# Performance work log

Hardware: AMD Instinct MI355X
Metric: run time of the kernel (lower is better)

The kernel has to match this reference:

```python
import jax, jax.numpy as jnp
import numpy as np

B, T, D, H = 32, 2048, 1024, 128


def setup_inputs() -> dict:
    key = jax.random.key(0)
    ks = jax.random.split(key, 7)
    s = 1.0 / np.sqrt(D)
    return {
        "x": jax.random.normal(ks[0], (B, T, D), dtype=jnp.float32),
        "Wk": jax.random.normal(ks[1], (D, H), dtype=jnp.float32) * s,
        "bk": jax.random.normal(ks[2], (H,), dtype=jnp.float32) * 0.01,
        "Wq": jax.random.normal(ks[3], (D, H), dtype=jnp.float32) * s,
        "bq": jax.random.normal(ks[4], (H,), dtype=jnp.float32) * 0.01,
        "Wv": jax.random.normal(ks[5], (D, H), dtype=jnp.float32) * s,
        "bv": jax.random.normal(ks[6], (H,), dtype=jnp.float32) * 0.01,
    }


def reference(x, Wk, bk, Wq, bq, Wv, bv):
    # Single causal attention head. NOTE faithful quirk: scores = K @ Q^T.
    k = x @ Wk + bk  # [B,T,H]
    q = x @ Wq + bq  # [B,T,H]
    v = x @ Wv + bv  # [B,T,H]
    scale = k.shape[-1] ** -0.5
    wei = jnp.einsum("bth,bsh->bts", k, q) * scale  # [B,T,T], K on the left
    t = x.shape[1]
    causal = jnp.tril(jnp.ones((t, t), dtype=bool))
    wei = jnp.where(causal, wei, -jnp.inf)
    wei = jax.nn.softmax(wei, axis=-1)
    # dropout is eval-mode identity (deterministic reference)
    out = jnp.einsum("bts,bsh->bth", wei, v)  # [B,T,H]
    return out
```

## Files before the change

kernel.cpp:

```cpp
#include <hip/hip_runtime.h>
#include <hip/hip_bf16.h>
#include <stdint.h>

typedef __bf16 bf16;
typedef __bf16 bf16x8 __attribute__((ext_vector_type(8)));
typedef __bf16 bf16x4 __attribute__((ext_vector_type(4)));
typedef float f32x4 __attribute__((ext_vector_type(4)));

#define BB 32
#define TT 2048
#define DD 1024
#define HH 128
#define SCALE 0.08838834764831845f
#define LOG2E 1.4426950408889634f

__device__ __forceinline__ void gl_lds16(const bf16* g, bf16* l) {
  __builtin_amdgcn_global_load_lds((__attribute__((address_space(1))) const void*)g,
                                   (__attribute__((address_space(3))) void*)l,
                                   16, 0, 0);
}

__global__ __launch_bounds__(256) void prep_w(const float* __restrict__ Wk,
                                              const float* __restrict__ Wq,
                                              const float* __restrict__ Wv,
                                              bf16* __restrict__ Wt) {
  int tid = blockIdx.x * 256 + threadIdx.x;
  int mat = tid >> 14;
  int r = tid & 16383;
  int h = r & 127;
  int d0 = (r >> 7) << 3;
  const float* W = (mat == 0) ? Wk : (mat == 1) ? Wq : Wv;
  bf16x8 v;
#pragma unroll
  for (int i = 0; i < 8; ++i) v[i] = (bf16)W[(size_t)(d0 + i) * HH + h];
  *(bf16x8*)(Wt + ((size_t)mat * HH + h) * DD + d0) = v;
}

__global__ __launch_bounds__(256) void qkv_proj(
    const float* __restrict__ x, const bf16* __restrict__ Wt,
    const float* __restrict__ bk, const float* __restrict__ bq,
    const float* __restrict__ bv,
    bf16* __restrict__ kb, bf16* __restrict__ qb, bf16* __restrict__ Vt) {
  const int bid = blockIdx.x;
  const int mat = bid % 3;
  const int mtile = bid / 3;
  const int tid = threadIdx.x;
  const int lane = tid & 63;
  const int w = tid >> 6;
  const int wr = w >> 1, wc = w & 1;
  const int l15 = lane & 15, l4 = lane >> 4;

  __shared__ __attribute__((aligned(16))) bf16 As[2][128][40];
  __shared__ __attribute__((aligned(16))) bf16 Bs[2][128][40];

  const size_t row0 = (size_t)mtile * 128;
  const bf16* Wm = Wt + (size_t)mat * HH * DD;
  const float* bias = (mat == 0) ? bk : (mat == 1) ? bq : bv;

  const int ar = tid >> 3, ac = (tid & 7) * 4;
  const int br = tid >> 2, bc = (tid & 3) * 8;

  f32x4 acc[4][4];
#pragma unroll
  for (int i = 0; i < 4; ++i)
#pragma unroll
    for (int j = 0; j < 4; ++j) acc[i][j] = f32x4{0.f, 0.f, 0.f, 0.f};

  auto stage = [&](int buf, int k0) {
#pragma unroll
    for (int p = 0; p < 4; ++p) {
      int r = p * 32 + ar;
      f32x4 a = *(const f32x4*)(x + (row0 + r) * DD + k0 + ac);
      bf16x4 t;
#pragma unroll
      for (int i = 0; i < 4; ++i) t[i] = (bf16)a[i];
      *(bf16x4*)&As[buf][r][ac] = t;
    }
#pragma unroll
    for (int p = 0; p < 2; ++p) {
      int r = p * 64 + br;
      bf16x8 bv8 = *(const bf16x8*)(Wm + (size_t)r * DD + k0 + bc);
      *(bf16x8*)&Bs[buf][r][bc] = bv8;
    }
  };

  stage(0, 0);
  __syncthreads();

  for (int k0 = 0; k0 < DD; k0 += 32) {
    const int cur = (k0 >> 5) & 1;
    if (k0 + 32 < DD) stage(cur ^ 1, k0 + 32);

    bf16x8 af[4], bfr[4];
#pragma unroll
    for (int f = 0; f < 4; ++f)
      af[f] = *(const bf16x8*)&As[cur][wr * 64 + f * 16 + l15][l4 * 8];
#pragma unroll
    for (int f = 0; f < 4; ++f)
      bfr[f] = *(const bf16x8*)&Bs[cur][wc * 64 + f * 16 + l15][l4 * 8];
#pragma unroll
    for (int i = 0; i < 4; ++i)
#pragma unroll
      for (int j = 0; j < 4; ++j)
        acc[i][j] = __builtin_amdgcn_mfma_f32_16x16x32_bf16(af[i], bfr[j],
                                                            acc[i][j], 0, 0, 0);
    __syncthreads();
  }

  float bvv[4];
#pragma unroll
  for (int f = 0; f < 4; ++f) bvv[f] = bias[wc * 64 + f * 16 + l15];

  if (mat == 2) {
    const int bidx = mtile >> 4;
    const int tbase = (mtile & 15) * 128;
#pragma unroll
    for (int i = 0; i < 4; ++i)
#pragma unroll
      for (int j = 0; j < 4; ++j) {
        int col = wc * 64 + j * 16 + l15;
        bf16x4 v4;
#pragma unroll
        for (int e = 0; e < 4; ++e) v4[e] = (bf16)(acc[i][j][e] + bvv[j]);
        int t = tbase + wr * 64 + i * 16 + l4 * 4;
        *(bf16x4*)(Vt + ((size_t)bidx * HH + col) * TT + t) = v4;
      }
  } else {
    const float ks = (mat == 0) ? (SCALE * LOG2E) : 1.0f;
    bf16* outp = (mat == 0) ? kb : qb;
#pragma unroll
    for (int i = 0; i < 4; ++i)
#pragma unroll
      for (int j = 0; j < 4; ++j) {
        int col = wc * 64 + j * 16 + l15;
#pragma unroll
        for (int e = 0; e < 4; ++e) {
          int row = wr * 64 + i * 16 + l4 * 4 + e;
          outp[(row0 + row) * HH + col] = (bf16)((acc[i][j][e] + bvv[j]) * ks);
        }
      }
  }
}

__global__ __launch_bounds__(256, 3) void attn(const bf16* __restrict__ kb,
                                               const bf16* __restrict__ qb,
                                               const bf16* __restrict__ Vt,
                                               float* __restrict__ out) {
  const int bid = blockIdx.x;
  const int b = bid & 31;
  const int p = bid >> 5;
  const int tid = threadIdx.x;
  const int lane = tid & 63;
  const int w = tid >> 6;
  const int l15 = lane & 15, l4 = lane >> 4;

  __shared__ __attribute__((aligned(16))) bf16 Es[64 * 128];
  __shared__ __attribute__((aligned(16))) bf16 Vs[128 * 64];
  __shared__ __attribute__((aligned(16))) bf16 Ps[4][16 * 72];

  for (int job = 0; job < 2; ++job) {
    const int tile = job ? p : (31 - p);
    const int t0 = tile * 64;

    bf16x8 af[4];
    {
      const bf16* kp = kb + ((size_t)b * TT + t0 + w * 16 + l15) * HH + l4 * 8;
#pragma unroll
      for (int kc = 0; kc < 4; ++kc) af[kc] = *(const bf16x8*)(kp + kc * 32);
    }

    f32x4 o[8];
#pragma unroll
    for (int j = 0; j < 8; ++j) o[j] = f32x4{0.f, 0.f, 0.f, 0.f};
    float mrow[4], lrow[4];
#pragma unroll
    for (int e = 0; e < 4; ++e) { mrow[e] = -1e30f; lrow[e] = 0.f; }

    const int nst = tile + 1;
    for (int jt = 0; jt < nst; ++jt) {
      const int s0 = jt * 64;
      {
        const bf16* Eg = qb + ((size_t)b * TT + s0) * HH;
#pragma unroll
        for (int it = 0; it < 4; ++it) {
          int L = w * 256 + it * 64 + lane;
          int er = L >> 4, ec = L & 15;
          int ecs = ec ^ (er & 7);
          gl_lds16(Eg + er * HH + ecs * 8, Es + (size_t)(w * 256 + it * 64) * 8);
        }
        const bf16* Vg = Vt + (size_t)b * HH * TT + s0;
#pragma unroll
        for (int it = 0; it < 4; ++it) {
          int L = w * 256 + it * 64 + lane;
          int vr = L >> 3, vc = L & 7;
          int vcs = vc ^ (vr & 7);
          gl_lds16(Vg + (size_t)vr * TT + vcs * 8, Vs + (size_t)(w * 256 + it * 64) * 8);
        }
      }
      __syncthreads();

      f32x4 s[4];
#pragma unroll
      for (int j = 0; j < 4; ++j) s[j] = f32x4{0.f, 0.f, 0.f, 0.f};
#pragma unroll
      for (int kc = 0; kc < 4; ++kc) {
        bf16x8 ef[4];
#pragma unroll
        for (int fn = 0; fn < 4; ++fn) {
          int er = fn * 16 + l15;
          int c = kc * 4 + l4;
          int cs = c ^ (er & 7);
          ef[fn] = *(const bf16x8*)&Es[er * 128 + cs * 8];
        }
#pragma unroll
        for (int fn = 0; fn < 4; ++fn)
          s[fn] = __builtin_amdgcn_mfma_f32_16x16x32_bf16(af[kc], ef[fn],
                                                          s[fn], 0, 0, 0);
      }

      if (s0 + 63 > t0 + w * 16) {
#pragma unroll
        for (int fn = 0; fn < 4; ++fn)
#pragma unroll
          for (int e = 0; e < 4; ++e) {
            int tg = t0 + w * 16 + l4 * 4 + e;
            int sg = s0 + fn * 16 + l15;
            if (sg > tg) s[fn][e] = -1e30f;
          }
      }

      float mx[4];
#pragma unroll
      for (int e = 0; e < 4; ++e) {
        float m = fmaxf(fmaxf(s[0][e], s[1][e]), fmaxf(s[2][e], s[3][e]));
#pragma unroll
        for (int d = 1; d < 16; d <<= 1) m = fmaxf(m, __shfl_xor(m, d));
        mx[e] = m;
      }
      float g = fmaxf(fmaxf(mx[0] - mrow[0], mx[1] - mrow[1]),
                      fmaxf(mx[2] - mrow[2], mx[3] - mrow[3]));
      if (!__all(g <= 8.0f)) {
#pragma unroll
        for (int e = 0; e < 4; ++e) {
          float mn = fmaxf(mrow[e], mx[e]);
          float rsc = exp2f(mrow[e] - mn);
          lrow[e] *= rsc;
#pragma unroll
          for (int fh = 0; fh < 8; ++fh) o[fh][e] *= rsc;
          mrow[e] = mn;
        }
      }
#pragma unroll
      for (int e = 0; e < 4; ++e) {
        float ps = 0.f;
#pragma unroll
        for (int fn = 0; fn < 4; ++fn) {
          float pv = exp2f(s[fn][e] - mrow[e]);
          s[fn][e] = pv;
          ps += pv;
        }
#pragma unroll
        for (int d = 1; d < 16; d <<= 1) ps += __shfl_xor(ps, d);
        lrow[e] += ps;
      }

#pragma unroll
      for (int fn = 0; fn < 4; ++fn)
#pragma unroll
        for (int e = 0; e < 4; ++e)
          Ps[w][(l4 * 4 + e) * 72 + fn * 16 + l15] = (bf16)s[fn][e];

#pragma unroll
      for (int kc = 0; kc < 2; ++kc) {
        bf16x8 pf = *(const bf16x8*)&Ps[w][l15 * 72 + kc * 32 + l4 * 8];
#pragma unroll
        for (int fh = 0; fh < 8; ++fh) {
          int vr = fh * 16 + l15;
          int c = kc * 4 + l4;
          int cs = c ^ (vr & 7);
          bf16x8 vf = *(const bf16x8*)&Vs[vr * 64 + cs * 8];
          o[fh] = __builtin_amdgcn_mfma_f32_16x16x32_bf16(pf, vf, o[fh], 0, 0, 0);
        }
      }
      __syncthreads();
    }

#pragma unroll
    for (int e = 0; e < 4; ++e) {
      float rl = 1.0f / lrow[e];
      int tg = t0 + w * 16 + l4 * 4 + e;
#pragma unroll
      for (int fh = 0; fh < 8; ++fh)
        out[((size_t)b * TT + tg) * HH + fh * 16 + l15] = o[fh][e] * rl;
    }
  }
}

extern "C" void kernel_launch(void* const* d_in, const int* in_sizes, int n_in,
                              void* d_out, int out_size, void* d_ws, size_t ws_size,
                              hipStream_t stream) {
  (void)in_sizes; (void)n_in; (void)out_size; (void)ws_size;
  const float* x  = (const float*)d_in[0];
  const float* Wk = (const float*)d_in[1];
  const float* bk = (const float*)d_in[2];
  const float* Wq = (const float*)d_in[3];
  const float* bq = (const float*)d_in[4];
  const float* Wv = (const float*)d_in[5];
  const float* bv = (const float*)d_in[6];
  float* out = (float*)d_out;

  const size_t NTH = (size_t)BB * TT * HH;
  bf16* kb = (bf16*)d_ws;
  bf16* qb = kb + NTH;
  bf16* Vt = qb + NTH;
  bf16* Wt = Vt + NTH;

  prep_w<<<192, 256, 0, stream>>>(Wk, Wq, Wv, Wt);
  qkv_proj<<<512 * 3, 256, 0, stream>>>(x, Wt, bk, bq, bv, kb, qb, Vt);
  attn<<<512, 256, 0, stream>>>(kb, qb, Vt, out);
}
```

Before: 226.1 us.

## Fuse QKV projections into one 64x384 tile, stream weights from global

The QKV projection kernel now computes all three outputs per block: each block takes 64 rows of x and produces 384 columns (K, Q and V concatenated), so x is read and converted to bf16 only once instead of three times. Weight fragments are loaded straight from global memory and x tiles are staged through an XOR-swizzled LDS buffer with register prefetch. The K scale is folded into the prepared weights and bias. The trade-offs are higher register pressure (24 accumulators per lane) and weight traffic going through L2 without LDS staging.

```diff
diff --git a/kernel.cpp b/kernel.cpp
--- a/kernel.cpp
+++ b/kernel.cpp
@@ -6,6 +6,7 @@
 typedef __bf16 bf16x8 __attribute__((ext_vector_type(8)));
 typedef __bf16 bf16x4 __attribute__((ext_vector_type(4)));
 typedef float f32x4 __attribute__((ext_vector_type(4)));
+typedef float f32x8 __attribute__((ext_vector_type(8)));
 
 #define BB 32
 #define TT 2048
@@ -13,6 +14,7 @@
 #define HH 128
 #define SCALE 0.08838834764831845f
 #define LOG2E 1.4426950408889634f
+#define KS (SCALE * LOG2E)
 
 __device__ __forceinline__ void gl_lds16(const bf16* g, bf16* l) {
   __builtin_amdgcn_global_load_lds((__attribute__((address_space(1))) const void*)g,
@@ -23,123 +25,133 @@
 __global__ __launch_bounds__(256) void prep_w(const float* __restrict__ Wk,
                                               const float* __restrict__ Wq,
                                               const float* __restrict__ Wv,
-                                              bf16* __restrict__ Wt) {
+                                              const float* __restrict__ bk,
+                                              const float* __restrict__ bq,
+                                              const float* __restrict__ bv,
+                                              bf16* __restrict__ Wt,
+                                              float* __restrict__ bcat) {
   int tid = blockIdx.x * 256 + threadIdx.x;
+  if (tid < 384) {
+    int mat = tid >> 7, h = tid & 127;
+    float bb = (mat == 0) ? bk[h] : (mat == 1) ? bq[h] : bv[h];
+    bcat[tid] = (mat == 0) ? bb * KS : bb;
+  }
   int mat = tid >> 14;
   int r = tid & 16383;
   int h = r & 127;
   int d0 = (r >> 7) << 3;
   const float* W = (mat == 0) ? Wk : (mat == 1) ? Wq : Wv;
+  const float ks = (mat == 0) ? KS : 1.0f;
   bf16x8 v;
 #pragma unroll
-  for (int i = 0; i < 8; ++i) v[i] = (bf16)W[(size_t)(d0 + i) * HH + h];
+  for (int i = 0; i < 8; ++i) v[i] = (bf16)(W[(size_t)(d0 + i) * HH + h] * ks);
   *(bf16x8*)(Wt + ((size_t)mat * HH + h) * DD + d0) = v;
 }
 
-__global__ __launch_bounds__(256) void qkv_proj(
+__global__ __launch_bounds__(256, 3) void qkv_proj(
     const float* __restrict__ x, const bf16* __restrict__ Wt,
-    const float* __restrict__ bk, const float* __restrict__ bq,
-    const float* __restrict__ bv,
+    const float* __restrict__ bcat,
     bf16* __restrict__ kb, bf16* __restrict__ qb, bf16* __restrict__ Vt) {
   const int bid = blockIdx.x;
-  const int mat = bid % 3;
-  const int mtile = bid / 3;
   const int tid = threadIdx.x;
   const int lane = tid & 63;
   const int w = tid >> 6;
-  const int wr = w >> 1, wc = w & 1;
   const int l15 = lane & 15, l4 = lane >> 4;
-
-  __shared__ __attribute__((aligned(16))) bf16 As[2][128][40];
-  __shared__ __attribute__((aligned(16))) bf16 Bs[2][128][40];
-
-  const size_t row0 = (size_t)mtile * 128;
-  const bf16* Wm = Wt + (size_t)mat * HH * DD;
-  const float* bias = (mat == 0) ? bk : (mat == 1) ? bq : bv;
-
-  const int ar = tid >> 3, ac = (tid & 7) * 4;
-  const int br = tid >> 2, bc = (tid & 3) * 8;
-
-  f32x4 acc[4][4];
-#pragma unroll
-  for (int i = 0; i < 4; ++i)
-#pragma unroll
-    for (int j = 0; j < 4; ++j) acc[i][j] = f32x4{0.f, 0.f, 0.f, 0.f};
-
-  auto stage = [&](int buf, int k0) {
-#pragma unroll
-    for (int p = 0; p < 4; ++p) {
-      int r = p * 32 + ar;
-      f32x4 a = *(const f32x4*)(x + (row0 + r) * DD + k0 + ac);
-      bf16x4 t;
-#pragma unroll
-      for (int i = 0; i < 4; ++i) t[i] = (bf16)a[i];
-      *(bf16x4*)&As[buf][r][ac] = t;
-    }
-#pragma unroll
-    for (int p = 0; p < 2; ++p) {
-      int r = p * 64 + br;
-      bf16x8 bv8 = *(const bf16x8*)(Wm + (size_t)r * DD + k0 + bc);
-      *(bf16x8*)&Bs[buf][r][bc] = bv8;
-    }
+  const size_t row0 = (size_t)bid * 64;
+  const int colbase = w * 96;
+
+  __shared__ __attribute__((aligned(16))) bf16 As[2][64][64];
+
+  const int sr0 = tid >> 3, sc0 = tid & 7;
+  const int sr1 = (256 + tid) >> 3, sc1 = tid & 7;
+
+  f32x4 acc[4][6];
+#pragma unroll
+  for (int m = 0; m < 4; ++m)
+#pragma unroll
+    for (int n = 0; n < 6; ++n) acc[m][n] = f32x4{0.f, 0.f, 0.f, 0.f};
+
+  auto cvt_store = [&](int buf, f32x8 a, int r, int c) {
+    bf16x8 t;
+#pragma unroll
+    for (int i = 0; i < 8; ++i) t[i] = (bf16)a[i];
+    *(bf16x8*)&As[buf][r][(c ^ (r & 7)) * 8] = t;
   };
 
-  stage(0, 0);
+  {
+    f32x8 a0 = *(const f32x8*)(x + (row0 + sr0) * DD + sc0 * 8);
+    f32x8 a1 = *(const f32x8*)(x + (row0 + sr1) * DD + sc1 * 8);
+    cvt_store(0, a0, sr0, sc0);
+    cvt_store(0, a1, sr1, sc1);
+  }
   __syncthreads();
 
-  for (int k0 = 0; k0 < DD; k0 += 32) {
-    const int cur = (k0 >> 5) & 1;
-    if (k0 + 32 < DD) stage(cur ^ 1, k0 + 32);
-
-    bf16x8 af[4], bfr[4];
-#pragma unroll
-    for (int f = 0; f < 4; ++f)
-      af[f] = *(const bf16x8*)&As[cur][wr * 64 + f * 16 + l15][l4 * 8];
-#pragma unroll
-    for (int f = 0; f < 4; ++f)
-      bfr[f] = *(const bf16x8*)&Bs[cur][wc * 64 + f * 16 + l15][l4 * 8];
-#pragma unroll
-    for (int i = 0; i < 4; ++i)
-#pragma unroll
-      for (int j = 0; j < 4; ++j)
-        acc[i][j] = __builtin_amdgcn_mfma_f32_16x16x32_bf16(af[i], bfr[j],
-                                                            acc[i][j], 0, 0, 0);
+  for (int step = 0; step < 16; ++step) {
+    const int k0 = step * 64;
+    const int cur = step & 1;
+
+    f32x8 n0, n1;
+    if (step < 15) {
+      n0 = *(const f32x8*)(x + (row0 + sr0) * DD + k0 + 64 + sc0 * 8);
+      n1 = *(const f32x8*)(x + (row0 + sr1) * DD + k0 + 64 + sc1 * 8);
+    }
+
+#pragma unroll
+    for (int kc = 0; kc < 2; ++kc) {
+      bf16x8 af[4];
+#pragma unroll
+      for (int m = 0; m < 4; ++m) {
+        int r = m * 16 + l15;
+        af[m] = *(const bf16x8*)&As[cur][r][((kc * 4 + l4) ^ (r & 7)) * 8];
+      }
+      bf16x8 bfr[6];
+#pragma unroll
+      for (int n = 0; n < 6; ++n)
+        bfr[n] = *(const bf16x8*)(Wt + (size_t)(colbase + n * 16 + l15) * DD +
+                                  k0 + kc * 32 + l4 * 8);
+#pragma unroll
+      for (int m = 0; m < 4; ++m)
+#pragma unroll
+        for (int n = 0; n < 6; ++n)
+          acc[m][n] = __builtin_amdgcn_mfma_f32_16x16x32_bf16(af[m], bfr[n],
+                                                              acc[m][n], 0, 0, 0);
+    }
+
+    if (step < 15) {
+      cvt_store(cur ^ 1, n0, sr0, sc0);
+      cvt_store(cur ^ 1, n1, sr1, sc1);
+    }
     __syncthreads();
   }
 
-  float bvv[4];
-#pragma unroll
-  for (int f = 0; f < 4; ++f) bvv[f] = bias[wc * 64 + f * 16 + l15];
-
-  if (mat == 2) {
-    const int bidx = mtile >> 4;
-    const int tbase = (mtile & 15) * 128;
-#pragma unroll
-    for (int i = 0; i < 4; ++i)
-#pragma unroll
-      for (int j = 0; j < 4; ++j) {
-        int col = wc * 64 + j * 16 + l15;
+  float bvv[6];
+#pragma unroll
+  for (int n = 0; n < 6; ++n) bvv[n] = bcat[colbase + n * 16 + l15];
+
+  const int bidx = bid >> 5;
+  const int tloc0 = (bid & 31) * 64;
+#pragma unroll
+  for (int m = 0; m < 4; ++m)
+#pragma unroll
+    for (int n = 0; n < 6; ++n) {
+      int col = colbase + n * 16 + l15;
+      int mat = col >> 7;
+      int hcol = col & 127;
+      if (mat == 2) {
         bf16x4 v4;
 #pragma unroll
-        for (int e = 0; e < 4; ++e) v4[e] = (bf16)(acc[i][j][e] + bvv[j]);
-        int t = tbase + wr * 64 + i * 16 + l4 * 4;
-        *(bf16x4*)(Vt + ((size_t)bidx * HH + col) * TT + t) = v4;
-      }
-  } else {
-    const float ks = (mat == 0) ? (SCALE * LOG2E) : 1.0f;
-    bf16* outp = (mat == 0) ? kb : qb;
-#pragma unroll
-    for (int i = 0; i < 4; ++i)
-#pragma unroll
-      for (int j = 0; j < 4; ++j) {
-        int col = wc * 64 + j * 16 + l15;
+        for (int e = 0; e < 4; ++e) v4[e] = (bf16)(acc[m][n][e] + bvv[n]);
+        int t = tloc0 + m * 16 + l4 * 4;
+        *(bf16x4*)(Vt + ((size_t)bidx * HH + hcol) * TT + t) = v4;
+      } else {
+        bf16* dst = (mat == 0) ? kb : qb;
 #pragma unroll
         for (int e = 0; e < 4; ++e) {
-          int row = wr * 64 + i * 16 + l4 * 4 + e;
-          outp[(row0 + row) * HH + col] = (bf16)((acc[i][j][e] + bvv[j]) * ks);
-        }
-      }
-  }
+          size_t rowg = row0 + m * 16 + l4 * 4 + e;
+          dst[rowg * HH + hcol] = (bf16)(acc[m][n][e] + bvv[n]);
+        }
+      }
+    }
 }
 
 __global__ __launch_bounds__(256, 3) void attn(const bf16* __restrict__ kb,
@@ -314,8 +326,9 @@
   bf16* qb = kb + NTH;
   bf16* Vt = qb + NTH;
   bf16* Wt = Vt + NTH;
-
-  prep_w<<<192, 256, 0, stream>>>(Wk, Wq, Wv, Wt);
-  qkv_proj<<<512 * 3, 256, 0, stream>>>(x, Wt, bk, bq, bv, kb, qb, Vt);
+  float* bcat = (float*)(Wt + (size_t)3 * HH * DD);
+
+  prep_w<<<192, 256, 0, stream>>>(Wk, Wq, Wv, bk, bq, bv, Wt, bcat);
+  qkv_proj<<<1024, 256, 0, stream>>>(x, Wt, bcat, kb, qb, Vt);
   attn<<<512, 256, 0, stream>>>(kb, qb, Vt, out);
 }
```

After: 254.3 us. 1.12x slower.
